# Kernel optimization log

Measured on AMD Instinct MI355X. Metric: run time of the kernel, lower is better.

Reference implementation:

```python
import jax, jax.numpy as jnp
import numpy as np

B, L, D = 4, 2048, 1024
H, DH = 16, 64  # heads, head dim (D = H*DH)


def setup_inputs() -> dict:
    key = jax.random.key(0)
    k1, k2, k3 = jax.random.split(key, 3)
    scale = D ** -0.5
    xin = jax.random.normal(k1, (B, L, D), dtype=jnp.float32)
    W_qkv = jax.random.normal(k2, (D, 3 * D), dtype=jnp.float32) * scale
    W_o = jax.random.normal(k3, (D, D), dtype=jnp.float32) * scale
    return {"xin": xin, "W_qkv": W_qkv, "W_o": W_o}


def reference(xin, W_qkv, W_o):
    b, Lq, _ = xin.shape
    # QKV projection: (b, L, 3D). NOTE: original torch code reshapes the
    # (b, L, 3D) buffer directly to (b, 3, H, L, DH) — a non-standard axis
    # interleave — which we replicate faithfully.
    QKV = (xin @ W_qkv).reshape(b, 3, H, Lq, DH)
    Q, K, V = QKV[:, 0], QKV[:, 1], QKV[:, 2]  # each (b, H, L, DH)
    scores = jnp.einsum("bhqd,bhkd->bhqk", Q, K) * (DH ** -0.5)
    attn = jax.nn.softmax(scores, axis=-1)  # dropout_prob=0.0 -> identity
    out = jnp.einsum("bhqk,bhkd->bhqd", attn, V)
    out = out.transpose(0, 2, 1, 3).reshape(b, Lq, H * DH)
    return out @ W_o
```

## Files before the change

### kernel.cpp

```cpp
#include <hip/hip_runtime.h>
#include <stdint.h>

typedef short short8 __attribute__((ext_vector_type(8)));
typedef float f32x4 __attribute__((ext_vector_type(4)));

#define LOG2E 1.44269504088896f
#define AS1 __attribute__((address_space(1)))
#define AS3 __attribute__((address_space(3)))

__device__ __forceinline__ float fexp2(float x) {
#if __has_builtin(__builtin_amdgcn_exp2f)
    return __builtin_amdgcn_exp2f(x);
#else
    return exp2f(x);
#endif
}
__device__ __forceinline__ unsigned short f2bfbits(float f) {
    unsigned x = __builtin_bit_cast(unsigned, f);
    unsigned r = x + 0x7fffu + ((x >> 16) & 1u);
    return (unsigned short)(r >> 16);
}
__device__ __forceinline__ float bfbits2f(unsigned short b) {
    unsigned u = ((unsigned)b) << 16;
    return __builtin_bit_cast(float, u);
}
__device__ __forceinline__ void unpack8(uint4 u, float4& f0, float4& f1) {
    f0.x = bfbits2f((unsigned short)(u.x & 0xffffu)); f0.y = bfbits2f((unsigned short)(u.x >> 16));
    f0.z = bfbits2f((unsigned short)(u.y & 0xffffu)); f0.w = bfbits2f((unsigned short)(u.y >> 16));
    f1.x = bfbits2f((unsigned short)(u.z & 0xffffu)); f1.y = bfbits2f((unsigned short)(u.z >> 16));
    f1.z = bfbits2f((unsigned short)(u.w & 0xffffu)); f1.w = bfbits2f((unsigned short)(u.w >> 16));
}
__device__ __forceinline__ unsigned pack2(float a, float b) {
    return (unsigned)f2bfbits(a) | ((unsigned)f2bfbits(b) << 16);
}
__device__ __forceinline__ void glds16(const void* gp, void* lp) {
    __builtin_amdgcn_global_load_lds((const AS1 unsigned*)(uintptr_t)gp,
                                     (AS3 unsigned*)(unsigned)(uintptr_t)lp, 16, 0, 0);
}

__global__ __launch_bounds__(256) void xbf_k(const float* __restrict__ x,
                                             unsigned short* __restrict__ y) {
    int i = (blockIdx.x * 256 + threadIdx.x) * 4;
    float4 v = *(const float4*)(x + i);
    uint2 u;
    u.x = pack2(v.x, v.y);
    u.y = pack2(v.z, v.w);
    *(uint2*)(y + i) = u;
}

__global__ __launch_bounds__(256) void t32cvt_k(const float* __restrict__ src,
                                                unsigned short* __restrict__ dst,
                                                int R, int C) {
    __shared__ float tile[32][36];
    int t = threadIdx.x;
    int bx = blockIdx.x, by = blockIdx.y;
    int r = t >> 3, c0 = (t & 7) * 4;
    *(float4*)&tile[r][c0] = *(const float4*)(src + (size_t)(by * 32 + r) * C + bx * 32 + c0);
    __syncthreads();
    uint2 u;
    u.x = pack2(tile[c0 + 0][r], tile[c0 + 1][r]);
    u.y = pack2(tile[c0 + 2][r], tile[c0 + 3][r]);
    *(uint2*)(dst + (size_t)(bx * 32 + r) * R + by * 32 + c0) = u;
}

template <bool CF32>
__global__ __launch_bounds__(256) void gemm_k(const unsigned short* __restrict__ A,
                                              const unsigned short* __restrict__ Bt,
                                              void* __restrict__ Cv,
                                              int M, int N, int K) {
    __shared__ unsigned short sA[128 * 32];
    __shared__ unsigned short sB[128 * 32];
    int t = threadIdx.x;
    int wid = t >> 6, lane = t & 63;
    int wm = (wid >> 1) * 64, wn = (wid & 1) * 64;
    int lm = lane & 15, lq = lane >> 4;
    size_t m0 = (size_t)blockIdx.y * 128, n0 = (size_t)blockIdx.x * 128;
    int srow = t >> 2, scol = (t & 3) * 8;
    const unsigned short* ga0 = A + (m0 + srow) * K + scol;
    const unsigned short* ga1 = A + (m0 + 64 + srow) * K + scol;
    const unsigned short* gb0 = Bt + (n0 + srow) * K + scol;
    const unsigned short* gb1 = Bt + (n0 + 64 + srow) * K + scol;
    unsigned short* laA0 = &sA[wid * 512];
    unsigned short* laA1 = &sA[2048 + wid * 512];
    unsigned short* laB0 = &sB[wid * 512];
    unsigned short* laB1 = &sB[2048 + wid * 512];
    f32x4 acc[4][4] = {};
    for (int k0 = 0; k0 < K; k0 += 32) {
        __syncthreads();
        glds16(ga0 + k0, laA0);
        glds16(ga1 + k0, laA1);
        glds16(gb0 + k0, laB0);
        glds16(gb1 + k0, laB1);
        __syncthreads();
        short8 af[4], bfr[4];
        #pragma unroll
        for (int i = 0; i < 4; ++i) af[i] = *(const short8*)&sA[(wm + i * 16 + lm) * 32 + lq * 8];
        #pragma unroll
        for (int j = 0; j < 4; ++j) bfr[j] = *(const short8*)&sB[(wn + j * 16 + lm) * 32 + lq * 8];
        #pragma unroll
        for (int i = 0; i < 4; ++i)
            #pragma unroll
            for (int j = 0; j < 4; ++j)
                acc[i][j] = __builtin_amdgcn_mfma_f32_16x16x32_bf16(af[i], bfr[j], acc[i][j], 0, 0, 0);
    }
    #pragma unroll
    for (int i = 0; i < 4; ++i)
        #pragma unroll
        for (int j = 0; j < 4; ++j)
            #pragma unroll
            for (int r = 0; r < 4; ++r) {
                size_t row = m0 + wm + i * 16 + lq * 4 + r;
                size_t col = n0 + wn + j * 16 + lm;
                if (CF32) ((float*)Cv)[row * N + col] = acc[i][j][r];
                else ((unsigned short*)Cv)[row * N + col] = f2bfbits(acc[i][j][r]);
            }
}

__global__ __launch_bounds__(256) void vt_k(const unsigned short* __restrict__ qkv,
                                            unsigned short* __restrict__ vt) {
    __shared__ unsigned short tile[64 * 72];
    int kt = blockIdx.x, bh = blockIdx.y;
    int b = bh >> 4, h = bh & 15;
    const unsigned short* Vp = qkv + (size_t)b * 6291456 + 4194304 + (size_t)h * 131072;
    int t = threadIdx.x;
    int row = t >> 2, cc = (t & 3) * 16;
    const unsigned short* src = Vp + (size_t)(kt * 64 + row) * 64 + cc;
    *(uint4*)&tile[row * 72 + cc] = *(const uint4*)src;
    *(uint4*)&tile[row * 72 + cc + 8] = *(const uint4*)(src + 8);
    __syncthreads();
    unsigned v[8];
    #pragma unroll
    for (int j = 0; j < 8; ++j) {
        unsigned short a = tile[(cc + 2 * j) * 72 + row];
        unsigned short bsh = tile[(cc + 2 * j + 1) * 72 + row];
        v[j] = (unsigned)a | ((unsigned)bsh << 16);
    }
    unsigned short* dst = vt + ((size_t)bh * 64 + row) * 2048 + kt * 64 + cc;
    *(uint4*)dst = make_uint4(v[0], v[1], v[2], v[3]);
    *(uint4*)(dst + 8) = make_uint4(v[4], v[5], v[6], v[7]);
}

__global__ __launch_bounds__(256, 2) void attn_mfma(const unsigned short* __restrict__ qkv,
                                                    const unsigned short* __restrict__ vt,
                                                    unsigned short* __restrict__ aout) {
    __shared__ unsigned short Ks[64 * 72];
    __shared__ unsigned short Vs[64 * 72];
    __shared__ unsigned short Ps[4 * 64 * 72];
    int bid = blockIdx.x;
    int qt = bid & 7, h = (bid >> 3) & 15, b = bid >> 7;
    int t = threadIdx.x;
    int wave = t >> 6, lane = t & 63, lm = lane & 15, quad = lane >> 4;
    const unsigned short* Qb = qkv + (size_t)b * 6291456 + (size_t)h * 131072;
    const unsigned short* Kb = Qb + 2097152;
    const unsigned short* Vtb = vt + (size_t)(b * 16 + h) * 131072;
    int q0 = qt * 256 + wave * 64;

    const float qs = 0.125f * LOG2E;
    short8 qf[4][2];
    #pragma unroll
    for (int i = 0; i < 4; ++i)
        #pragma unroll
        for (int c = 0; c < 2; ++c) {
            uint4 u = *(const uint4*)(Qb + (size_t)(q0 + i * 16 + lm) * 64 + c * 32 + quad * 8);
            float4 f0, f1; unpack8(u, f0, f1);
            uint4 v;
            v.x = pack2(f0.x * qs, f0.y * qs);
            v.y = pack2(f0.z * qs, f0.w * qs);
            v.z = pack2(f1.x * qs, f1.y * qs);
            v.w = pack2(f1.z * qs, f1.w * qs);
            qf[i][c] = *(short8*)&v;
        }

    short8 ones;
    #pragma unroll
    for (int z = 0; z < 8; ++z) ones[z] = (short)0x3F80;

    f32x4 o[4][4] = {};
    f32x4 l_acc[4] = {};

    int srow = t >> 2, scol = (t & 3) * 16;
    unsigned short* psw = Ps + wave * 4608;

    for (int kt = 0; kt < 32; ++kt) {
        const unsigned short* kp = Kb + (size_t)(kt * 64 + srow) * 64 + scol;
        uint4 k0 = *(const uint4*)kp;
        uint4 k1 = *(const uint4*)(kp + 8);
        const unsigned short* vp = Vtb + (size_t)srow * 2048 + kt * 64 + scol;
        uint4 v0 = *(const uint4*)vp;
        uint4 v1 = *(const uint4*)(vp + 8);
        __syncthreads();
        *(uint4*)&Ks[srow * 72 + scol] = k0;
        *(uint4*)&Ks[srow * 72 + scol + 8] = k1;
        *(uint4*)&Vs[srow * 72 + scol] = v0;
        *(uint4*)&Vs[srow * 72 + scol + 8] = v1;
        __syncthreads();

        #pragma unroll
        for (int j = 0; j < 4; ++j) {
            short8 kf0 = *(const short8*)&Ks[(j * 16 + lm) * 72 + quad * 8];
            short8 kf1 = *(const short8*)&Ks[(j * 16 + lm) * 72 + 32 + quad * 8];
            f32x4 sf[4];
            #pragma unroll
            for (int i = 0; i < 4; ++i) {
                sf[i] = (f32x4){0.f, 0.f, 0.f, 0.f};
                sf[i] = __builtin_amdgcn_mfma_f32_16x16x32_bf16(qf[i][0], kf0, sf[i], 0, 0, 0);
                sf[i] = __builtin_amdgcn_mfma_f32_16x16x32_bf16(qf[i][1], kf1, sf[i], 0, 0, 0);
            }
            #pragma unroll
            for (int i = 0; i < 4; ++i)
                #pragma unroll
                for (int r = 0; r < 4; ++r) {
                    float p = fexp2(sf[i][r]);
                    unsigned bits = __builtin_bit_cast(unsigned, p);
                    psw[(i * 16 + quad * 4 + r) * 72 + j * 16 + lm] = (unsigned short)(bits >> 16);
                }
        }
        __syncthreads();

        #pragma unroll
        for (int c = 0; c < 2; ++c) {
            short8 pf[4];
            #pragma unroll
            for (int i = 0; i < 4; ++i)
                pf[i] = *(const short8*)&psw[(i * 16 + lm) * 72 + c * 32 + quad * 8];
            #pragma unroll
            for (int jd = 0; jd < 4; ++jd) {
                short8 vf = *(const short8*)&Vs[(jd * 16 + lm) * 72 + c * 32 + quad * 8];
                #pragma unroll
                for (int i = 0; i < 4; ++i)
                    o[i][jd] = __builtin_amdgcn_mfma_f32_16x16x32_bf16(pf[i], vf, o[i][jd], 0, 0, 0);
            }
            #pragma unroll
            for (int i = 0; i < 4; ++i)
                l_acc[i] = __builtin_amdgcn_mfma_f32_16x16x32_bf16(pf[i], ones, l_acc[i], 0, 0, 0);
        }
    }
    #pragma unroll
    for (int i = 0; i < 4; ++i)
        #pragma unroll
        for (int r = 0; r < 4; ++r) {
            float inv = 1.f / l_acc[i][r];
            int q = q0 + i * 16 + quad * 4 + r;
            size_t rowbase = ((size_t)b * 2048 + q) * 1024 + h * 64;
            #pragma unroll
            for (int jd = 0; jd < 4; ++jd)
                aout[rowbase + jd * 16 + lm] = f2bfbits(o[i][jd][r] * inv);
        }
}

extern "C" void kernel_launch(void* const* d_in, const int* in_sizes, int n_in,
                              void* d_out, int out_size, void* d_ws, size_t ws_size,
                              hipStream_t stream) {
    const float* xin  = (const float*)d_in[0];
    const float* wqkv = (const float*)d_in[1];
    const float* wo   = (const float*)d_in[2];
    float* out = (float*)d_out;

    char* ws = (char*)d_ws;
    unsigned short* qkv   = (unsigned short*)(ws);
    unsigned short* attn  = (unsigned short*)(ws + 50331648);
    unsigned short* wqkvT = (unsigned short*)(ws + 67108864);
    unsigned short* woT   = (unsigned short*)(ws + 73400320);
    unsigned short* vt    = (unsigned short*)(ws + 75497472);
    unsigned short* xb    = (unsigned short*)(ws + 92274688);

    dim3 blk(256);
    xbf_k<<<dim3(8192), blk, 0, stream>>>(xin, xb);
    t32cvt_k<<<dim3(3072 / 32, 1024 / 32), blk, 0, stream>>>(wqkv, wqkvT, 1024, 3072);
    t32cvt_k<<<dim3(1024 / 32, 1024 / 32), blk, 0, stream>>>(wo, woT, 1024, 1024);
    gemm_k<false><<<dim3(3072 / 128, 8192 / 128), blk, 0, stream>>>(xb, wqkvT, qkv, 8192, 3072, 1024);
    vt_k<<<dim3(32, 64), blk, 0, stream>>>(qkv, vt);
    attn_mfma<<<dim3(512), blk, 0, stream>>>(qkv, vt, attn);
    gemm_k<true><<<dim3(1024 / 128, 8192 / 128), blk, 0, stream>>>(attn, woT, out, 8192, 1024, 1024);
}
```

Before: 299.6 us.

## Swap MFMA operand order to produce transposed P and vectorize P/output stores

```diff
diff --git a/kernel.cpp b/kernel.cpp
--- a/kernel.cpp
+++ b/kernel.cpp
@@ -32,6 +32,9 @@
 }
 __device__ __forceinline__ unsigned pack2(float a, float b) {
     return (unsigned)f2bfbits(a) | ((unsigned)f2bfbits(b) << 16);
+}
+__device__ __forceinline__ unsigned tpack2(float a, float b) {
+    return (__builtin_bit_cast(unsigned, a) >> 16) | (__builtin_bit_cast(unsigned, b) & 0xffff0000u);
 }
 __device__ __forceinline__ void glds16(const void* gp, void* lp) {
     __builtin_amdgcn_global_load_lds((const AS1 unsigned*)(uintptr_t)gp,
@@ -145,7 +148,7 @@
                                                     unsigned short* __restrict__ aout) {
     __shared__ unsigned short Ks[64 * 72];
     __shared__ unsigned short Vs[64 * 72];
-    __shared__ unsigned short Ps[4 * 64 * 72];
+    __shared__ unsigned short Ps[4 * 64 * 68];
     int bid = blockIdx.x;
     int qt = bid & 7, h = (bid >> 3) & 15, b = bid >> 7;
     int t = threadIdx.x;
@@ -179,7 +182,7 @@
     f32x4 l_acc[4] = {};
 
     int srow = t >> 2, scol = (t & 3) * 16;
-    unsigned short* psw = Ps + wave * 4608;
+    unsigned short* psw = Ps + wave * 4352;
 
     for (int kt = 0; kt < 32; ++kt) {
         const unsigned short* kp = Kb + (size_t)(kt * 64 + srow) * 64 + scol;
@@ -199,53 +202,51 @@
         for (int j = 0; j < 4; ++j) {
             short8 kf0 = *(const short8*)&Ks[(j * 16 + lm) * 72 + quad * 8];
             short8 kf1 = *(const short8*)&Ks[(j * 16 + lm) * 72 + 32 + quad * 8];
-            f32x4 sf[4];
             #pragma unroll
             for (int i = 0; i < 4; ++i) {
-                sf[i] = (f32x4){0.f, 0.f, 0.f, 0.f};
-                sf[i] = __builtin_amdgcn_mfma_f32_16x16x32_bf16(qf[i][0], kf0, sf[i], 0, 0, 0);
-                sf[i] = __builtin_amdgcn_mfma_f32_16x16x32_bf16(qf[i][1], kf1, sf[i], 0, 0, 0);
+                f32x4 sf = {0.f, 0.f, 0.f, 0.f};
+                sf = __builtin_amdgcn_mfma_f32_16x16x32_bf16(kf0, qf[i][0], sf, 0, 0, 0);
+                sf = __builtin_amdgcn_mfma_f32_16x16x32_bf16(kf1, qf[i][1], sf, 0, 0, 0);
+                float p0 = fexp2(sf[0]), p1 = fexp2(sf[1]);
+                float p2 = fexp2(sf[2]), p3 = fexp2(sf[3]);
+                uint2 w;
+                w.x = tpack2(p0, p1);
+                w.y = tpack2(p2, p3);
+                *(uint2*)&psw[(i * 16 + lm) * 68 + j * 16 + quad * 4] = w;
             }
-            #pragma unroll
-            for (int i = 0; i < 4; ++i)
-                #pragma unroll
-                for (int r = 0; r < 4; ++r) {
-                    float p = fexp2(sf[i][r]);
-                    unsigned bits = __builtin_bit_cast(unsigned, p);
-                    psw[(i * 16 + quad * 4 + r) * 72 + j * 16 + lm] = (unsigned short)(bits >> 16);
-                }
-        }
-        __syncthreads();
+        }
 
         #pragma unroll
         for (int c = 0; c < 2; ++c) {
             short8 pf[4];
             #pragma unroll
             for (int i = 0; i < 4; ++i)
-                pf[i] = *(const short8*)&psw[(i * 16 + lm) * 72 + c * 32 + quad * 8];
+                pf[i] = *(const short8*)&psw[(i * 16 + lm) * 68 + c * 32 + quad * 8];
             #pragma unroll
             for (int jd = 0; jd < 4; ++jd) {
                 short8 vf = *(const short8*)&Vs[(jd * 16 + lm) * 72 + c * 32 + quad * 8];
                 #pragma unroll
                 for (int i = 0; i < 4; ++i)
-                    o[i][jd] = __builtin_amdgcn_mfma_f32_16x16x32_bf16(pf[i], vf, o[i][jd], 0, 0, 0);
+                    o[jd][i] = __builtin_amdgcn_mfma_f32_16x16x32_bf16(vf, pf[i], o[jd][i], 0, 0, 0);
             }
             #pragma unroll
             for (int i = 0; i < 4; ++i)
-                l_acc[i] = __builtin_amdgcn_mfma_f32_16x16x32_bf16(pf[i], ones, l_acc[i], 0, 0, 0);
-        }
-    }
-    #pragma unroll
-    for (int i = 0; i < 4; ++i)
-        #pragma unroll
-        for (int r = 0; r < 4; ++r) {
-            float inv = 1.f / l_acc[i][r];
-            int q = q0 + i * 16 + quad * 4 + r;
-            size_t rowbase = ((size_t)b * 2048 + q) * 1024 + h * 64;
-            #pragma unroll
-            for (int jd = 0; jd < 4; ++jd)
-                aout[rowbase + jd * 16 + lm] = f2bfbits(o[i][jd][r] * inv);
-        }
+                l_acc[i] = __builtin_amdgcn_mfma_f32_16x16x32_bf16(ones, pf[i], l_acc[i], 0, 0, 0);
+        }
+    }
+    #pragma unroll
+    for (int i = 0; i < 4; ++i) {
+        float inv = 1.f / l_acc[i][0];
+        size_t row = (size_t)b * 2048 + q0 + i * 16 + lm;
+        unsigned short* op = aout + row * 1024 + h * 64 + quad * 4;
+        #pragma unroll
+        for (int jd = 0; jd < 4; ++jd) {
+            uint2 u;
+            u.x = pack2(o[jd][i][0] * inv, o[jd][i][1] * inv);
+            u.y = pack2(o[jd][i][2] * inv, o[jd][i][3] * inv);
+            *(uint2*)(op + jd * 16) = u;
+        }
+    }
 }
 
 extern "C" void kernel_launch(void* const* d_in, const int* in_sizes, int n_in,
```

New measurement: 326.9 us. 9.1% more time.
